# Kernel tuning notes

Hardware: AMD Instinct MI355X
Metric: run time of the kernel (lower is better)

The kernel has to match this reference:

```python
import jax, jax.numpy as jnp
import numpy as np

SUB1 = 0.5
SUB2 = 0.2


def setup_inputs() -> dict:
    key = jax.random.key(0)
    k1, k2, k3 = jax.random.split(key, 3)
    x = jax.random.normal(k1, (32, 64, 128, 128), dtype=jnp.float32)
    conv_weight = jax.random.normal(k2, (128, 64, 3, 3), dtype=jnp.float32) * 0.05
    conv_bias = jax.random.normal(k3, (128,), dtype=jnp.float32) * 0.05
    return {"x": x, "conv_weight": conv_weight, "conv_bias": conv_bias}


def reference(x, conv_weight, conv_bias):
    # Conv2d, stride 1, VALID padding (kernel computes out_h = in_h - K + 1)
    y = jax.lax.conv_general_dilated(
        x, conv_weight,
        window_strides=(1, 1), padding="VALID",
        dimension_numbers=("NCHW", "OIHW", "NCHW"))
    y = y + conv_bias[None, :, None, None]
    v = y - SUB1 - SUB2
    # Mish: v * tanh(softplus(v)); softplus == log(1 + exp(v)) (stable form)
    return v * jnp.tanh(jax.nn.softplus(v))
```

## Files before the change

### kernel.cpp

```cpp
#include <hip/hip_runtime.h>
#include <hip/hip_bf16.h>

typedef short bf16x8 __attribute__((ext_vector_type(8)));
typedef float f32x4 __attribute__((ext_vector_type(4)));

constexpr int C_IN = 64, H_IN = 128, W_IN = 128, C_OUT = 128, OH = 126, OW = 126;
constexpr int PAD = 72;
constexpr float SUBC = 0.7f;

__global__ void reorder_weights(const float* __restrict__ w, __hip_bfloat16* __restrict__ wr) {
    int o = blockIdx.x * 256 + threadIdx.x;
    if (o >= 9 * C_OUT * C_IN) return;
    int ci = o & 63;
    int co = (o >> 6) & 127;
    int k9 = o >> 13;
    int kh = k9 / 3, kw = k9 % 3;
    wr[o] = __float2bfloat16(w[((co * C_IN + ci) * 3 + kh) * 3 + kw]);
}

__global__ __launch_bounds__(256, 2) void conv_mish(
    const float* __restrict__ x, const __hip_bfloat16* __restrict__ wr,
    const float* __restrict__ bias, float* __restrict__ out)
{
    __shared__ __hip_bfloat16 Xs[128 * PAD];
    __shared__ __hip_bfloat16 Bs[128 * PAD];

    int b = blockIdx.x;
    int lb = (b & 7) * 504 + (b >> 3);
    int n  = lb / OH;
    int oh = lb % OH;

    int tid  = threadIdx.x;
    int lane = tid & 63;
    int wv   = tid >> 6;
    int wm   = wv >> 1;
    int wn   = wv & 1;
    int quad = lane >> 4;
    int l16  = lane & 15;

    f32x4 acc[4][4] = {};

    const float* xn = x + (size_t)n * C_IN * H_IN * W_IN;

    for (int kh = 0; kh < 3; ++kh) {
        __syncthreads();
        {
            int h   = oh + kh;
            int w4  = (tid & 31) * 4;
            int cib = tid >> 5;
            for (int r = 0; r < 8; ++r) {
                int ci = cib + r * 8;
                float4 v = *(const float4*)(xn + ((size_t)ci * H_IN + h) * W_IN + w4);
                Xs[(w4 + 0) * PAD + ci] = __float2bfloat16(v.x);
                Xs[(w4 + 1) * PAD + ci] = __float2bfloat16(v.y);
                Xs[(w4 + 2) * PAD + ci] = __float2bfloat16(v.z);
                Xs[(w4 + 3) * PAD + ci] = __float2bfloat16(v.w);
            }
        }
        for (int kw = 0; kw < 3; ++kw) {
            if (kw) __syncthreads();
            {
                const __hip_bfloat16* src = wr + ((kh * 3 + kw) << 13);
                for (int r = 0; r < 4; ++r) {
                    int c   = tid + r * 256;
                    int co  = c >> 3;
                    int ci8 = (c & 7) << 3;
                    *(bf16x8*)&Bs[co * PAD + ci8] = *(const bf16x8*)(src + co * 64 + ci8);
                }
            }
            __syncthreads();
            for (int half = 0; half < 2; ++half) {
                int k0 = half * 32 + quad * 8;
                bf16x8 a[4], bf[4];
                for (int i = 0; i < 4; ++i) {
                    int m = wm * 64 + i * 16 + l16;
                    int widx = m + kw; if (widx > 127) widx = 127;
                    a[i] = *(const bf16x8*)&Xs[widx * PAD + k0];
                }
                for (int j = 0; j < 4; ++j) {
                    int co = wn * 64 + j * 16 + l16;
                    bf[j] = *(const bf16x8*)&Bs[co * PAD + k0];
                }
                for (int i = 0; i < 4; ++i)
                    for (int j = 0; j < 4; ++j)
                        acc[i][j] = __builtin_amdgcn_mfma_f32_16x16x32_bf16(a[i], bf[j], acc[i][j], 0, 0, 0);
            }
        }
    }

    for (int j = 0; j < 4; ++j) {
        int co = wn * 64 + j * 16 + l16;
        float bb = bias[co] - SUBC;
        for (int i = 0; i < 4; ++i) {
            int ow0 = wm * 64 + i * 16 + quad * 4;
            float o[4];
            for (int r = 0; r < 4; ++r) {
                float v = acc[i][j][r] + bb;
                float e = __expf(v);
                float t = e * (e + 2.0f);
                float m = v * t * __builtin_amdgcn_rcpf(t + 2.0f);
                o[r] = (v > 20.0f) ? v : m;
            }
            float* dst = out + (((size_t)n * C_OUT + co) * OH + oh) * OW + ow0;
            float2 p0; p0.x = o[0]; p0.y = o[1];
            *(float2*)dst = p0;
            if (ow0 + 2 < OW) {
                float2 p1; p1.x = o[2]; p1.y = o[3];
                *(float2*)(dst + 2) = p1;
            }
        }
    }
}

extern "C" void kernel_launch(void* const* d_in, const int* in_sizes, int n_in,
                              void* d_out, int out_size, void* d_ws, size_t ws_size,
                              hipStream_t stream) {
    const float* x    = (const float*)d_in[0];
    const float* w    = (const float*)d_in[1];
    const float* bias = (const float*)d_in[2];
    float* out        = (float*)d_out;
    __hip_bfloat16* wr = (__hip_bfloat16*)d_ws;

    reorder_weights<<<(9 * C_OUT * C_IN + 255) / 256, 256, 0, stream>>>(w, wr);
    conv_mish<<<32 * OH, 256, 0, stream>>>(x, wr, bias, out);
}
```

Measured before the change: 450.1 us.

## Load MFMA weight fragments directly from global memory and vectorize X staging

Weights are pre-reordered into the per-lane MFMA fragment layout, so each wave reads its B operands straight from global memory (served from L2) instead of staging them through shared memory. This drops the weight LDS buffer and two barriers per kw step. The X tile staging now uses float2 loads across 16 channels per wave and writes packed bf16x8 vectors to LDS, replacing scalar bf16 stores. Launch bounds are raised to allow three blocks per CU, at the risk of register pressure and more global weight traffic per block.

Result: no change. 455.3 us (+1.2%).

```diff
diff --git a/kernel.cpp b/kernel.cpp
--- a/kernel.cpp
+++ b/kernel.cpp
@@ -5,27 +5,30 @@
 typedef float f32x4 __attribute__((ext_vector_type(4)));
 
 constexpr int C_IN = 64, H_IN = 128, W_IN = 128, C_OUT = 128, OH = 126, OW = 126;
-constexpr int PAD = 72;
+constexpr int XPAD = 72;
 constexpr float SUBC = 0.7f;
 
-__global__ void reorder_weights(const float* __restrict__ w, __hip_bfloat16* __restrict__ wr) {
+__global__ void reorder_weights(const float* __restrict__ w, __hip_bfloat16* __restrict__ wr2) {
     int o = blockIdx.x * 256 + threadIdx.x;
-    if (o >= 9 * C_OUT * C_IN) return;
-    int ci = o & 63;
-    int co = (o >> 6) & 127;
-    int k9 = o >> 13;
+    if (o >= 9 * 2 * 8 * 64 * 8) return;
+    int jj   = o & 7;
+    int lane = (o >> 3) & 63;
+    int jt   = (o >> 9) & 7;
+    int half = (o >> 12) & 1;
+    int k9   = o >> 13;
+    int co = jt * 16 + (lane & 15);
+    int ci = half * 32 + (lane >> 4) * 8 + jj;
     int kh = k9 / 3, kw = k9 % 3;
-    wr[o] = __float2bfloat16(w[((co * C_IN + ci) * 3 + kh) * 3 + kw]);
+    wr2[o] = __float2bfloat16(w[((co * C_IN + ci) * 3 + kh) * 3 + kw]);
 }
 
-__global__ __launch_bounds__(256, 2) void conv_mish(
-    const float* __restrict__ x, const __hip_bfloat16* __restrict__ wr,
+__global__ __launch_bounds__(256, 3) void conv_mish(
+    const float* __restrict__ x, const __hip_bfloat16* __restrict__ wr2,
     const float* __restrict__ bias, float* __restrict__ out)
 {
-    __shared__ __hip_bfloat16 Xs[128 * PAD];
-    __shared__ __hip_bfloat16 Bs[128 * PAD];
+    __shared__ __hip_bfloat16 Xs[128 * XPAD];
 
-    int b = blockIdx.x;
+    int b  = blockIdx.x;
     int lb = (b & 7) * 504 + (b >> 3);
     int n  = lb / OH;
     int oh = lb % OH;
@@ -45,45 +48,51 @@
     for (int kh = 0; kh < 3; ++kh) {
         __syncthreads();
         {
-            int h   = oh + kh;
-            int w4  = (tid & 31) * 4;
-            int cib = tid >> 5;
-            for (int r = 0; r < 8; ++r) {
-                int ci = cib + r * 8;
-                float4 v = *(const float4*)(xn + ((size_t)ci * H_IN + h) * W_IN + w4);
-                Xs[(w4 + 0) * PAD + ci] = __float2bfloat16(v.x);
-                Xs[(w4 + 1) * PAD + ci] = __float2bfloat16(v.y);
-                Xs[(w4 + 2) * PAD + ci] = __float2bfloat16(v.z);
-                Xs[(w4 + 3) * PAD + ci] = __float2bfloat16(v.w);
+            int h  = oh + kh;
+            int cB = wv;
+            const float2* src = (const float2*)(xn + ((size_t)(cB * 16) * H_IN + h) * W_IN) + lane;
+            float2 ld[16];
+            #pragma unroll
+            for (int j = 0; j < 16; ++j) ld[j] = src[(size_t)j * (H_IN * W_IN / 2)];
+            #pragma unroll
+            for (int sw = 0; sw < 2; ++sw) {
+                #pragma unroll
+                for (int sc = 0; sc < 2; ++sc) {
+                    bf16x8 v;
+                    #pragma unroll
+                    for (int jj = 0; jj < 8; ++jj) {
+                        float f = sw ? ld[sc * 8 + jj].y : ld[sc * 8 + jj].x;
+                        __hip_bfloat16 hbf = __float2bfloat16(f);
+                        v[jj] = *(short*)&hbf;
+                    }
+                    *(bf16x8*)&Xs[(2 * lane + sw) * XPAD + (2 * cB + sc) * 8] = v;
+                }
             }
         }
+        __syncthreads();
+        #pragma unroll 1
         for (int kw = 0; kw < 3; ++kw) {
-            if (kw) __syncthreads();
-            {
-                const __hip_bfloat16* src = wr + ((kh * 3 + kw) << 13);
-                for (int r = 0; r < 4; ++r) {
-                    int c   = tid + r * 256;
-                    int co  = c >> 3;
-                    int ci8 = (c & 7) << 3;
-                    *(bf16x8*)&Bs[co * PAD + ci8] = *(const bf16x8*)(src + co * 64 + ci8);
-                }
-            }
-            __syncthreads();
+            const __hip_bfloat16* wb = wr2 + (size_t)(kh * 3 + kw) * 8192;
+            #pragma unroll
             for (int half = 0; half < 2; ++half) {
                 int k0 = half * 32 + quad * 8;
-                bf16x8 a[4], bf[4];
+                bf16x8 a[4], bw[4];
+                #pragma unroll
+                for (int j = 0; j < 4; ++j) {
+                    int jt = wn * 4 + j;
+                    bw[j] = *(const bf16x8*)(wb + ((half * 8 + jt) * 64 + lane) * 8);
+                }
+                #pragma unroll
                 for (int i = 0; i < 4; ++i) {
                     int m = wm * 64 + i * 16 + l16;
                     int widx = m + kw; if (widx > 127) widx = 127;
-                    a[i] = *(const bf16x8*)&Xs[widx * PAD + k0];
+                    a[i] = *(const bf16x8*)&Xs[widx * XPAD + k0];
                 }
-                for (int j = 0; j < 4; ++j) {
-                    int co = wn * 64 + j * 16 + l16;
-                    bf[j] = *(const bf16x8*)&Bs[co * PAD + k0];
-                }
+                #pragma unroll
                 for (int i = 0; i < 4; ++i)
+                    #pragma unroll
                     for (int j = 0; j < 4; ++j)
-                        acc[i][j] = __builtin_amdgcn_mfma_f32_16x16x32_bf16(a[i], bf[j], acc[i][j], 0, 0, 0);
+                        acc[i][j] = __builtin_amdgcn_mfma_f32_16x16x32_bf16(a[i], bw[j], acc[i][j], 0, 0, 0);
             }
         }
     }
@@ -119,8 +128,8 @@
     const float* w    = (const float*)d_in[1];
     const float* bias = (const float*)d_in[2];
     float* out        = (float*)d_out;
-    __hip_bfloat16* wr = (__hip_bfloat16*)d_ws;
+    __hip_bfloat16* wr2 = (__hip_bfloat16*)d_ws;
 
-    reorder_weights<<<(9 * C_OUT * C_IN + 255) / 256, 256, 0, stream>>>(w, wr);
-    conv_mish<<<32 * OH, 256, 0, stream>>>(x, wr, bias, out);
+    reorder_weights<<<(73728 + 255) / 256, 256, 0, stream>>>(w, wr2);
+    conv_mish<<<32 * OH, 256, 0, stream>>>(x, wr2, bias, out);
 }
```
